# Kernel optimization log

Measured on AMD Instinct MI355X. Metric: run time of the kernel, lower is better.

## Reference

```python
import jax, jax.numpy as jnp
import numpy as np

BATCH = 256
INPUT_DIM = 512
OUTPUT_DIM = 512
NUM_WORKERS = 512
TOP_K = 154


def setup_inputs() -> dict:
    key = jax.random.key(0)
    k_x, k_gw, k_t = jax.random.split(key, 3)
    x = jax.random.normal(k_x, (BATCH, INPUT_DIM), dtype=jnp.float32)
    # router gate: nn.Linear(input_dim, num_workers), weight ~ N(0, 0.01), bias = 0
    gate_w = jax.random.normal(k_gw, (NUM_WORKERS, INPUT_DIM), dtype=jnp.float32) * 0.01
    gate_b = jnp.zeros((NUM_WORKERS,), dtype=jnp.float32)
    # 512 worker tiles, each [output_dim, input_dim], init randn*0.01
    tiles = jax.random.normal(k_t, (NUM_WORKERS, OUTPUT_DIM, INPUT_DIM), dtype=jnp.float32) * 0.01
    return {"x": x, "gate_w": gate_w, "gate_b": gate_b, "tiles": tiles}


def reference(x, gate_w, gate_b, tiles):
    B = x.shape[0]
    # Router: logits -> top-k -> softmax over selected scores
    gate_logits = x @ gate_w.T + gate_b                      # [B, E]
    scores, indices = jax.lax.top_k(gate_logits, TOP_K)      # [B, K]
    weights = jax.nn.softmax(scores, axis=-1)                # [B, K]
    # Scatter top-k weights into a dense [B, E] combine matrix (rest zero).
    w_full = jnp.zeros((B, NUM_WORKERS), dtype=x.dtype)
    w_full = w_full.at[jnp.arange(B)[:, None], indices].add(weights)
    # weight * (x @ tile.T) == (weight * x) @ tile.T  (linearity), so scale
    # inputs per (token, expert) and contract against all expert tiles.
    xw = w_full[:, :, None] * x[:, None, :]                  # [B, E, D]
    output = jnp.einsum('bed,eod->bo', xw, tiles)            # [B, O]
    return output
```

## Files before the change

### kernel.cpp

```cpp
#include <hip/hip_runtime.h>
#include <hip/hip_bf16.h>

#define B_ 256
#define D_ 512
#define E_ 512
#define K_ 154

typedef __attribute__((ext_vector_type(8))) short short8;
typedef __attribute__((ext_vector_type(4))) float f32x4;

__device__ __forceinline__ unsigned short f2bf(float f) {
    unsigned u = __float_as_uint(f);
    u = (u + 0x7fffu + ((u >> 16) & 1u)) >> 16;
    return (unsigned short)u;
}

__device__ __forceinline__ unsigned cvt_pk_bf16(float a, float b) {
    unsigned r;
    asm("v_cvt_pk_bf16_f32 %0, %1, %2" : "=v"(r) : "v"(a), "v"(b));
    return r;
}

__device__ __forceinline__ short8 pack_bf16x8(f32x4 a, f32x4 b) {
    union { unsigned u[4]; short8 s; } r;
    r.u[0] = cvt_pk_bf16(a.x, a.y);
    r.u[1] = cvt_pk_bf16(a.z, a.w);
    r.u[2] = cvt_pk_bf16(b.x, b.y);
    r.u[3] = cvt_pk_bf16(b.z, b.w);
    return r.s;
}

__global__ __launch_bounds__(512) void k_gate(const float* __restrict__ x,
                                              const float* __restrict__ gw,
                                              double* __restrict__ logits) {
    const int tg = blockIdx.x;
    const int eg = blockIdx.y;
    const int tid = threadIdx.x;
    const int t0 = tg * 8, e0 = eg * 64;
    __shared__ double xs[8][512];
    __shared__ float gws[64][65];
    #pragma unroll
    for (int i = 0; i < 8; ++i) {
        int j = i * 512 + tid;
        xs[j >> 9][j & 511] = (double)x[(t0 + (j >> 9)) * D_ + (j & 511)];
    }
    const int e = tid & 63, tl = tid >> 6;
    double acc = 0.0;
    for (int dc = 0; dc < 8; ++dc) {
        __syncthreads();
        #pragma unroll
        for (int i = 0; i < 8; ++i) {
            int j = i * 512 + tid;
            gws[j >> 6][j & 63] = gw[(e0 + (j >> 6)) * D_ + dc * 64 + (j & 63)];
        }
        __syncthreads();
        #pragma unroll 8
        for (int d = 0; d < 64; ++d)
            acc = fma((double)gws[e][d], xs[tl][dc * 64 + d], acc);
    }
    logits[(t0 + tl) * E_ + e0 + e] = acc;
}

__global__ __launch_bounds__(512) void k_topk(const double* __restrict__ logits,
                                              const float* __restrict__ gb,
                                              const float* __restrict__ x,
                                              float* __restrict__ wT,
                                              unsigned short* __restrict__ xb) {
    const int b = blockIdx.x;
    const int e = threadIdx.x;
    __shared__ double vals[E_];
    __shared__ double red[512];
    double v = logits[b * E_ + e] + (double)gb[e];
    vals[e] = v;
    xb[b * D_ + e] = f2bf(x[b * D_ + e]);
    __syncthreads();
    int cnt = 0;
    double m = -1.0e300;
    for (int j = 0; j < E_; ++j) {
        double vj = vals[j];
        m = fmax(m, vj);
        cnt += (vj > v || (vj == v && j < e)) ? 1 : 0;
    }
    double p = (cnt < K_) ? exp(v - m) : 0.0;
    red[e] = p;
    __syncthreads();
    for (int s = 256; s > 0; s >>= 1) {
        if (e < s) red[e] += red[e + s];
        __syncthreads();
    }
    wT[e * B_ + b] = (float)(p / red[0]);
}

template <int EPG, bool TWO>
__global__ __launch_bounds__(256, 2) void k_moe(const unsigned short* __restrict__ xb,
                                                const float* __restrict__ wT,
                                                const float* __restrict__ tiles,
                                                float* __restrict__ dst) {
    const int nt = blockIdx.x & 15;
    const int g  = blockIdx.x >> 4;
    const int n0 = nt * 32;
    const int e0 = g * EPG;
    const int tid  = threadIdx.x;
    const int wv   = tid >> 6;
    const int lane = tid & 63;
    const int m0   = wv * 64;
    const int quad = lane >> 4;
    const int l16  = lane & 15;

    __shared__ float ws[EPG][B_];
    #pragma unroll
    for (int i = 0; i < EPG; ++i) {
        int idx = i * 256 + tid;
        ws[idx >> 8][idx & 255] = wT[(e0 + (idx >> 8)) * B_ + (idx & 255)];
    }
    __syncthreads();

    f32x4 Ct[4][2];
    #pragma unroll
    for (int mi = 0; mi < 4; ++mi)
        #pragma unroll
        for (int ni = 0; ni < 2; ++ni)
            Ct[mi][ni] = (f32x4){0.f, 0.f, 0.f, 0.f};

    const float* bp0 = tiles + ((size_t)e0 * D_ + n0 + l16) * D_ + quad * 8;

    for (int kc = 0; kc < 8; ++kc) {
        const int k0 = kc * 64;
        short8 A[4][2];
        #pragma unroll
        for (int mi = 0; mi < 4; ++mi)
            #pragma unroll
            for (int ks = 0; ks < 2; ++ks)
                A[mi][ks] = *(const short8*)&xb[(m0 + mi * 16 + l16) * D_ + k0 + ks * 32 + quad * 8];

        const float* pk = bp0 + k0;
        #pragma unroll 2
        for (int e = 0; e < EPG; ++e) {
            const float* pe = pk + (size_t)e * (D_ * D_);
            f32x4 Ce[4][2];
            #pragma unroll
            for (int mi = 0; mi < 4; ++mi)
                #pragma unroll
                for (int ni = 0; ni < 2; ++ni)
                    Ce[mi][ni] = (f32x4){0.f, 0.f, 0.f, 0.f};
            #pragma unroll
            for (int ks = 0; ks < 2; ++ks) {
                short8 Bf[2];
                #pragma unroll
                for (int ni = 0; ni < 2; ++ni) {
                    const float* q = pe + ni * (16 * D_) + ks * 32;
                    f32x4 u = *(const f32x4*)q;
                    f32x4 v = *(const f32x4*)(q + 4);
                    Bf[ni] = pack_bf16x8(u, v);
                }
                #pragma unroll
                for (int mi = 0; mi < 4; ++mi)
                    #pragma unroll
                    for (int ni = 0; ni < 2; ++ni)
                        Ce[mi][ni] = __builtin_amdgcn_mfma_f32_16x16x32_bf16(
                            A[mi][ks], Bf[ni], Ce[mi][ni], 0, 0, 0);
            }
            const float* wrow = ws[e];
            #pragma unroll
            for (int mi = 0; mi < 4; ++mi) {
                const int rbase = m0 + mi * 16 + quad * 4;
                float w0 = wrow[rbase + 0], w1 = wrow[rbase + 1];
                float w2 = wrow[rbase + 2], w3 = wrow[rbase + 3];
                #pragma unroll
                for (int ni = 0; ni < 2; ++ni) {
                    Ct[mi][ni].x += w0 * Ce[mi][ni].x;
                    Ct[mi][ni].y += w1 * Ce[mi][ni].y;
                    Ct[mi][ni].z += w2 * Ce[mi][ni].z;
                    Ct[mi][ni].w += w3 * Ce[mi][ni].w;
                }
            }
        }
    }
    #pragma unroll
    for (int mi = 0; mi < 4; ++mi)
        #pragma unroll
        for (int ni = 0; ni < 2; ++ni) {
            const int row = m0 + mi * 16 + quad * 4;
            const int col = n0 + ni * 16 + l16;
            if (TWO) {
                float* base = dst + ((size_t)g * B_ + row) * D_ + col;
                __builtin_nontemporal_store(Ct[mi][ni].x, base + 0 * D_);
                __builtin_nontemporal_store(Ct[mi][ni].y, base + 1 * D_);
                __builtin_nontemporal_store(Ct[mi][ni].z, base + 2 * D_);
                __builtin_nontemporal_store(Ct[mi][ni].w, base + 3 * D_);
            } else {
                unsafeAtomicAdd(&dst[(row + 0) * D_ + col], Ct[mi][ni].x);
                unsafeAtomicAdd(&dst[(row + 1) * D_ + col], Ct[mi][ni].y);
                unsafeAtomicAdd(&dst[(row + 2) * D_ + col], Ct[mi][ni].z);
                unsafeAtomicAdd(&dst[(row + 3) * D_ + col], Ct[mi][ni].w);
            }
        }
}

template <int NG>
__global__ __launch_bounds__(256) void k_reduce(const float* __restrict__ P,
                                                float* __restrict__ out) {
    const int t = blockIdx.x * 256 + threadIdx.x;
    const f32x4* p4 = (const f32x4*)P;
    f32x4 acc = (f32x4){0.f, 0.f, 0.f, 0.f};
    #pragma unroll 8
    for (int gidx = 0; gidx < NG; ++gidx) {
        f32x4 v = __builtin_nontemporal_load(p4 + (size_t)gidx * 32768 + t);
        acc.x += v.x; acc.y += v.y; acc.z += v.z; acc.w += v.w;
    }
    ((f32x4*)out)[t] = acc;
}

extern "C" void kernel_launch(void* const* d_in, const int* in_sizes, int n_in,
                              void* d_out, int out_size, void* d_ws, size_t ws_size,
                              hipStream_t stream) {
    const float* x     = (const float*)d_in[0];
    const float* gw    = (const float*)d_in[1];
    const float* gb    = (const float*)d_in[2];
    const float* tiles = (const float*)d_in[3];
    float* out = (float*)d_out;

    char* base = (char*)d_ws;
    unsigned short* xb  = (unsigned short*)base;
    float* wT           = (float*)(base + 262144);
    double* logits      = (double*)(base + 262144 + 524288);
    float* P            = (float*)(base + 262144 + 524288);
    const size_t fixed  = 262144 + 524288;
    const size_t slot   = (size_t)B_ * D_ * sizeof(float);
    const size_t need16 = fixed + 32 * slot;
    const size_t need32 = fixed + 16 * slot;

    k_gate<<<dim3(32, 8), 512, 0, stream>>>(x, gw, logits);
    k_topk<<<256, 512, 0, stream>>>(logits, gb, x, wT, xb);
    if (ws_size >= need16) {
        k_moe<16, true><<<512, 256, 0, stream>>>(xb, wT, tiles, P);
        k_reduce<32><<<128, 256, 0, stream>>>(P, out);
    } else if (ws_size >= need32) {
        k_moe<32, true><<<256, 256, 0, stream>>>(xb, wT, tiles, P);
        k_reduce<16><<<128, 256, 0, stream>>>(P, out);
    } else {
        hipMemsetAsync(out, 0, (size_t)out_size * sizeof(float), stream);
        k_moe<8, false><<<1024, 256, 0, stream>>>(xb, wT, tiles, out);
    }
}
```

Before: 896.5 us.

## Stage expert tile chunks into LDS with async global_load_lds double buffering

Replaces the direct per-lane global loads of fp32 expert tile fragments with a double-buffered LDS staging scheme. Each wave asynchronously copies one expert's 32x64 tile chunk into shared memory via global_load_lds, and the XOR swizzle avoids bank conflicts on the readback. The loads for the next step are issued while the current step's MFMAs run. This adds a 64KB LDS buffer and a barrier per step, which may reduce occupancy and adds synchronization cost.

```diff
diff --git a/kernel.cpp b/kernel.cpp
--- a/kernel.cpp
+++ b/kernel.cpp
@@ -8,6 +8,9 @@
 
 typedef __attribute__((ext_vector_type(8))) short short8;
 typedef __attribute__((ext_vector_type(4))) float f32x4;
+
+#define AS1 __attribute__((address_space(1)))
+#define AS3 __attribute__((address_space(3)))
 
 __device__ __forceinline__ unsigned short f2bf(float f) {
     unsigned u = __float_as_uint(f);
@@ -106,14 +109,35 @@
     const int m0   = wv * 64;
     const int quad = lane >> 4;
     const int l16  = lane & 15;
-
+    constexpr int PSTEPS = EPG / 4;
+    constexpr int NSTEP  = 8 * PSTEPS;
+
+    __shared__ __align__(16) float Bs[2][4][32][64];
     __shared__ float ws[EPG][B_];
+
     #pragma unroll
     for (int i = 0; i < EPG; ++i) {
         int idx = i * 256 + tid;
         ws[idx >> 8][idx & 255] = wT[(e0 + (idx >> 8)) * B_ + (idx & 255)];
     }
-    __syncthreads();
+
+    const int rl = lane >> 4;
+    const int pc = lane & 15;
+    auto stage = [&](int buf, int step) {
+        const int kc = step / PSTEPS, p = step % PSTEPS;
+        const int eg = e0 + p * 4 + wv;
+        const float* rowbase = tiles + ((size_t)eg * D_ + n0) * D_ + kc * 64;
+        float* dbase = &Bs[buf][wv][0][0];
+        #pragma unroll
+        for (int i = 0; i < 8; ++i) {
+            const int r = i * 4 + rl;
+            const int c = ((((pc >> 1) ^ (r & 7)) << 1) | (pc & 1));
+            const float* src = rowbase + (size_t)r * D_ + c * 4;
+            __builtin_amdgcn_global_load_lds((const AS1 void*)src,
+                                             (AS3 void*)(dbase + i * 256),
+                                             16, 0, 0);
+        }
+    };
 
     f32x4 Ct[4][2];
     #pragma unroll
@@ -122,7 +146,9 @@
         for (int ni = 0; ni < 2; ++ni)
             Ct[mi][ni] = (f32x4){0.f, 0.f, 0.f, 0.f};
 
-    const float* bp0 = tiles + ((size_t)e0 * D_ + n0 + l16) * D_ + quad * 8;
+    stage(0, 0);
+    __syncthreads();
+    int cur = 0;
 
     for (int kc = 0; kc < 8; ++kc) {
         const int k0 = kc * 64;
@@ -133,49 +159,59 @@
             for (int ks = 0; ks < 2; ++ks)
                 A[mi][ks] = *(const short8*)&xb[(m0 + mi * 16 + l16) * D_ + k0 + ks * 32 + quad * 8];
 
-        const float* pk = bp0 + k0;
-        #pragma unroll 2
-        for (int e = 0; e < EPG; ++e) {
-            const float* pe = pk + (size_t)e * (D_ * D_);
-            f32x4 Ce[4][2];
+        #pragma unroll
+        for (int p = 0; p < PSTEPS; ++p) {
+            const int step = kc * PSTEPS + p;
+            if (step + 1 < NSTEP) stage(cur ^ 1, step + 1);
+
             #pragma unroll
-            for (int mi = 0; mi < 4; ++mi)
-                #pragma unroll
-                for (int ni = 0; ni < 2; ++ni)
-                    Ce[mi][ni] = (f32x4){0.f, 0.f, 0.f, 0.f};
-            #pragma unroll
-            for (int ks = 0; ks < 2; ++ks) {
-                short8 Bf[2];
-                #pragma unroll
-                for (int ni = 0; ni < 2; ++ni) {
-                    const float* q = pe + ni * (16 * D_) + ks * 32;
-                    f32x4 u = *(const f32x4*)q;
-                    f32x4 v = *(const f32x4*)(q + 4);
-                    Bf[ni] = pack_bf16x8(u, v);
-                }
+            for (int el = 0; el < 4; ++el) {
+                const float* bsrc = &Bs[cur][el][0][0];
+                f32x4 Ce[4][2];
                 #pragma unroll
                 for (int mi = 0; mi < 4; ++mi)
                     #pragma unroll
                     for (int ni = 0; ni < 2; ++ni)
-                        Ce[mi][ni] = __builtin_amdgcn_mfma_f32_16x16x32_bf16(
-                            A[mi][ks], Bf[ni], Ce[mi][ni], 0, 0, 0);
-            }
-            const float* wrow = ws[e];
-            #pragma unroll
-            for (int mi = 0; mi < 4; ++mi) {
-                const int rbase = m0 + mi * 16 + quad * 4;
-                float w0 = wrow[rbase + 0], w1 = wrow[rbase + 1];
-                float w2 = wrow[rbase + 2], w3 = wrow[rbase + 3];
+                        Ce[mi][ni] = (f32x4){0.f, 0.f, 0.f, 0.f};
                 #pragma unroll
-                for (int ni = 0; ni < 2; ++ni) {
-                    Ct[mi][ni].x += w0 * Ce[mi][ni].x;
-                    Ct[mi][ni].y += w1 * Ce[mi][ni].y;
-                    Ct[mi][ni].z += w2 * Ce[mi][ni].z;
-                    Ct[mi][ni].w += w3 * Ce[mi][ni].w;
+                for (int ks = 0; ks < 2; ++ks) {
+                    short8 Bf[2];
+                    #pragma unroll
+                    for (int ni = 0; ni < 2; ++ni) {
+                        const int r  = ni * 16 + l16;
+                        const int ph = (((ks * 4 + quad) ^ (r & 7)) << 1);
+                        const float* q = bsrc + r * 64 + ph * 4;
+                        f32x4 u = *(const f32x4*)q;
+                        f32x4 v = *(const f32x4*)(q + 4);
+                        Bf[ni] = pack_bf16x8(u, v);
+                    }
+                    #pragma unroll
+                    for (int mi = 0; mi < 4; ++mi)
+                        #pragma unroll
+                        for (int ni = 0; ni < 2; ++ni)
+                            Ce[mi][ni] = __builtin_amdgcn_mfma_f32_16x16x32_bf16(
+                                A[mi][ks], Bf[ni], Ce[mi][ni], 0, 0, 0);
+                }
+                const float* wrow = ws[p * 4 + el];
+                #pragma unroll
+                for (int mi = 0; mi < 4; ++mi) {
+                    const int rbase = m0 + mi * 16 + quad * 4;
+                    float w0 = wrow[rbase + 0], w1 = wrow[rbase + 1];
+                    float w2 = wrow[rbase + 2], w3 = wrow[rbase + 3];
+                    #pragma unroll
+                    for (int ni = 0; ni < 2; ++ni) {
+                        Ct[mi][ni].x += w0 * Ce[mi][ni].x;
+                        Ct[mi][ni].y += w1 * Ce[mi][ni].y;
+                        Ct[mi][ni].z += w2 * Ce[mi][ni].z;
+                        Ct[mi][ni].w += w3 * Ce[mi][ni].w;
+                    }
                 }
             }
-        }
-    }
+            __syncthreads();
+            cur ^= 1;
+        }
+    }
+
     #pragma unroll
     for (int mi = 0; mi < 4; ++mi)
         #pragma unroll
```

After: 1.549 ms. 72.7% more time.
